# Optimization experiments

Measured on AMD Instinct MI355X. Metric: run time of the kernel, lower is better.

Reference implementation:

```python
import jax, jax.numpy as jnp
import numpy as np

N = 50000        # nodes
E = 1_600_000    # edges
G = 64           # graphs in batch
IN = 10          # raw node feature width
XS, XE = 4, 10   # bus slice -> in_dim = 6
H = 256          # hidden_dim
OUT = 256        # out_dim
L = 3            # n_layers per expert
NE = 8           # n_experts
K = 2            # top_k


def _w(key, shape):
    fan_in = shape[-2] if len(shape) > 1 else shape[-1]
    return jax.random.normal(key, shape, jnp.float32) / np.sqrt(fan_in).astype(np.float32)


def setup_inputs() -> dict:
    key = jax.random.key(0)
    ks = jax.random.split(key, 18)
    x = jax.random.normal(ks[0], (N, IN), jnp.float32)
    edge_index = jax.random.randint(ks[1], (2, E), 0, N, dtype=jnp.int32)
    batch = jnp.sort(jax.random.randint(ks[2], (N,), 0, G, dtype=jnp.int32))
    return {
        "x": x,
        "edge_index": edge_index,
        "batch": batch,
        # SharedBusEncoder: Linear(in_dim, hidden) + ReLU
        "W_enc": _w(ks[3], (XE - XS, H)), "b_enc": jnp.zeros((H,), jnp.float32),
        # semantic BaseRouter: Linear(H,H)+ReLU+Linear(H,NE)
        "Ws1": _w(ks[4], (H, H)), "bs1": jnp.zeros((H,), jnp.float32),
        "Ws2": _w(ks[5], (H, NE)), "bs2": jnp.zeros((NE,), jnp.float32),
        # structural BaseRouter: Linear(2,H)+ReLU+Linear(H,NE)
        "Wt1": _w(ks[6], (2, H)), "bt1": jnp.zeros((H,), jnp.float32),
        "Wt2": _w(ks[7], (H, NE)), "bt2": jnp.zeros((NE,), jnp.float32),
        # GraphConvExpert stacks: x' = x@W_self + (sum_neighbors x)@W_neigh + b
        "W_self": _w(ks[8], (NE, L, H, OUT)),
        "W_neigh": _w(ks[9], (NE, L, H, OUT)),
        "b_exp": jnp.zeros((NE, L, OUT), jnp.float32),
    }


def reference(x, edge_index, batch, W_enc, b_enc, Ws1, bs1, Ws2, bs2,
              Wt1, bt1, Wt2, bt2, W_self, W_neigh, b_exp):
    src, dst = edge_index[0], edge_index[1]

    # SharedBusEncoder on bus feature slice
    h = jax.nn.relu(x[:, XS:XE] @ W_enc + b_enc)                       # [N, H]

    # graph_size_features: per-graph log node/edge counts, broadcast to nodes
    nodes_per_g = jax.ops.segment_sum(jnp.ones((N,), jnp.float32), batch, G)
    edges_per_g = jax.ops.segment_sum(jnp.ones((E,), jnp.float32), batch[src], G)
    size_feat = jnp.stack([jnp.log1p(nodes_per_g), jnp.log1p(edges_per_g)], -1)[batch]  # [N, 2]

    # dual routers, averaged
    sem = jax.nn.relu(h @ Ws1 + bs1) @ Ws2 + bs2                       # [N, NE]
    stru = jax.nn.relu(size_feat @ Wt1 + bt1) @ Wt2 + bt2              # [N, NE]
    logits = 0.5 * sem + 0.5 * stru

    # sparse_routing: softmax -> top-k mask -> renormalize (eval path, no noise)
    probs = jax.nn.softmax(logits, axis=-1)
    _, topi = jax.lax.top_k(probs, K)                                  # [N, K]
    mask = jnp.zeros_like(probs).at[jnp.arange(N)[:, None], topi].set(1.0)
    sp = probs * mask
    sparse = sp / jnp.sum(sp, axis=-1, keepdims=True)                  # [N, NE]

    # dense GraphConv experts over all nodes
    def run_expert(Ws, Wn, b):
        z = h
        for l in range(L):
            agg = jax.ops.segment_sum(z[src], dst, N)                  # neighbor sum
            z = z @ Ws[l] + agg @ Wn[l] + b[l]
            if l < L - 1:
                z = jax.nn.relu(z)
        return z                                                        # [N, OUT]

    y = jax.vmap(run_expert)(W_self, W_neigh, b_exp)                   # [NE, N, OUT]
    return jnp.einsum('end,ne->nd', y, sparse)                         # [N, OUT]
```

## Files before the change

### kernel.cpp

```cpp
#include <hip/hip_runtime.h>
#include <hip/hip_bf16.h>


#define NN 50000
#define EE 1600000
#define GG 64
#define HH 256
#define NEXP 8
#define LAY 3
#define KD 512
#define MT 128
#define BK 64
#define LST 72

typedef __attribute__((ext_vector_type(8))) short bf16x8;
typedef __attribute__((ext_vector_type(8))) unsigned short u16x8;
typedef __attribute__((ext_vector_type(4))) float f32x4;

__device__ __forceinline__ float bf2f(unsigned short u) {
    union { unsigned int i; float f; } v; v.i = ((unsigned int)u) << 16; return v.f;
}
__device__ __forceinline__ unsigned short f2bf(float f) {
    union { unsigned int i; float f; } v; v.f = f;
    unsigned int r = (v.i + 0x7FFFu + ((v.i >> 16) & 1u)) >> 16;
    return (unsigned short)r;
}

__global__ void encoder_kernel(const float* __restrict__ x, const float* __restrict__ W,
                               const float* __restrict__ b, unsigned short* __restrict__ out) {
    int n = blockIdx.x, j = threadIdx.x;
    float acc = b[j];
#pragma unroll
    for (int i = 0; i < 6; i++) acc += x[n * 10 + 4 + i] * W[i * HH + j];
    acc = fmaxf(acc, 0.f);
    out[(long)n * KD + j] = f2bf(acc);
}

__global__ void pack_experts(const float* __restrict__ Wself, const float* __restrict__ Wneigh,
                             unsigned short* __restrict__ Bt) {
    int idx = blockIdx.x * 256 + threadIdx.x;
    int n = idx & 255; int r = idx >> 8;
    int k = r & 511; r >>= 9;
    int l = r % LAY; int e = r / LAY;
    float v = (k < 256) ? Wself[(((e * LAY + l) * HH) + k) * HH + n]
                        : Wneigh[(((e * LAY + l) * HH) + (k - 256)) * HH + n];
    Bt[(((long)(e * LAY + l) * HH + n) * KD) + k] = f2bf(v);
}

__global__ void pack_ws1(const float* __restrict__ W, unsigned short* __restrict__ Bt) {
    int idx = blockIdx.x * 256 + threadIdx.x;
    int n = idx & 255; int k = idx >> 8;
    Bt[(long)n * HH + k] = f2bf(W[k * HH + n]);
}

__global__ void deg_kernel(const int* __restrict__ src, const int* __restrict__ dst,
                           int* __restrict__ deg, int* __restrict__ outdeg) {
    int e = blockIdx.x * 256 + threadIdx.x;
    if (e < EE) {
        atomicAdd(&deg[dst[e]], 1);
        atomicAdd(&outdeg[src[e]], 1);
    }
}

__global__ void hist_kernel(const int* __restrict__ batch, const int* __restrict__ outdeg,
                            int* __restrict__ ncnt, int* __restrict__ ecnt) {
    __shared__ int hn[GG], he[GG];
    if (threadIdx.x < GG) { hn[threadIdx.x] = 0; he[threadIdx.x] = 0; }
    __syncthreads();
    int i = blockIdx.x * 256 + threadIdx.x;
    if (i < NN) {
        int g = batch[i];
        atomicAdd(&hn[g], 1);
        atomicAdd(&he[g], outdeg[i]);
    }
    __syncthreads();
    if (threadIdx.x < GG) {
        if (hn[threadIdx.x]) atomicAdd(&ncnt[threadIdx.x], hn[threadIdx.x]);
        if (he[threadIdx.x]) atomicAdd(&ecnt[threadIdx.x], he[threadIdx.x]);
    }
}

__global__ void stru_kernel(const int* __restrict__ ncnt, const int* __restrict__ ecnt,
                            const float* __restrict__ Wt1, const float* __restrict__ bt1,
                            const float* __restrict__ Wt2, const float* __restrict__ bt2,
                            float* __restrict__ strug) {
    __shared__ float t[HH];
    int g = blockIdx.x, j = threadIdx.x;
    float nf = log1pf((float)ncnt[g]);
    float ef = log1pf((float)ecnt[g]);
    float v = nf * Wt1[j] + ef * Wt1[HH + j] + bt1[j];
    t[j] = fmaxf(v, 0.f);
    __syncthreads();
    if (j < 8) {
        float sum = bt2[j];
        for (int k = 0; k < HH; k++) sum += t[k] * Wt2[k * 8 + j];
        strug[g * 8 + j] = sum;
    }
}

__global__ void scan_kernel(const int* __restrict__ deg, int* __restrict__ rowstart,
                            int* __restrict__ cursor) {
    __shared__ int wsum[16];
    __shared__ int carry_s;
    int tid = threadIdx.x;
    int wid = tid >> 6, lane = tid & 63;
    if (tid == 0) carry_s = 0;
    __syncthreads();
    for (int base = 0; base < NN; base += 1024) {
        int i = base + tid;
        int v = (i < NN) ? deg[i] : 0;
        int sc = v;
#pragma unroll
        for (int off = 1; off < 64; off <<= 1) {
            int t = __shfl_up(sc, off, 64);
            if (lane >= off) sc += t;
        }
        if (lane == 63) wsum[wid] = sc;
        __syncthreads();
        int carry = carry_s;
        int prev = 0;
        for (int w = 0; w < wid; w++) prev += wsum[w];
        int excl = carry + prev + sc - v;
        if (i < NN) { rowstart[i] = excl; cursor[i] = excl; }
        __syncthreads();
        if (tid == 1023) carry_s = carry + prev + sc;
    }
    __syncthreads();
    if (tid == 0) rowstart[NN] = carry_s;
}

__global__ void scatter_kernel(const int* __restrict__ src, const int* __restrict__ dst,
                               int* __restrict__ cursor, unsigned short* __restrict__ cols) {
    int e = blockIdx.x * 256 + threadIdx.x;
    if (e < EE) {
        int p = atomicAdd(&cursor[dst[e]], 1);
        cols[p] = (unsigned short)src[e];
    }
}

__global__ void agg_kernel(const unsigned short* __restrict__ Z, unsigned short* __restrict__ Aout,
                           const int* __restrict__ rowstart, const unsigned short* __restrict__ cols,
                           const int* __restrict__ list, const int* __restrict__ cntp) {
    int half = threadIdx.x >> 5;
    int lane = threadIdx.x & 31;
    int idx = blockIdx.x * 8 + half;
    int limit = cntp ? *cntp : NN;
    if (idx >= limit) return;
    int nid = list ? list[idx] : idx;
    int s = rowstart[nid], e = rowstart[nid + 1];
    float acc[8] = {0.f, 0.f, 0.f, 0.f, 0.f, 0.f, 0.f, 0.f};
    int i = s;
    for (; i + 8 <= e; i += 8) {
        int c[8];
#pragma unroll
        for (int u = 0; u < 8; u++) c[u] = (int)cols[i + u];
        u16x8 v[8];
#pragma unroll
        for (int u = 0; u < 8; u++) v[u] = *(const u16x8*)&Z[(long)c[u] * KD + lane * 8];
#pragma unroll
        for (int u = 0; u < 8; u++)
#pragma unroll
            for (int j = 0; j < 8; j++) acc[j] += bf2f(v[u][j]);
    }
    for (; i < e; i++) {
        int c = (int)cols[i];
        u16x8 v = *(const u16x8*)&Z[(long)c * KD + lane * 8];
#pragma unroll
        for (int j = 0; j < 8; j++) acc[j] += bf2f(v[j]);
    }
    u16x8 o;
#pragma unroll
    for (int j = 0; j < 8; j++) o[j] = f2bf(acc[j]);
    *(u16x8*)&Aout[(long)nid * KD + 256 + lane * 8] = o;
}

__global__ void route_kernel(const unsigned short* __restrict__ T, const float* __restrict__ Ws2,
                             const float* __restrict__ bs2, const float* __restrict__ strug,
                             const int* __restrict__ batch, float* __restrict__ sparse) {
    int nid = blockIdx.x * 4 + (threadIdx.x >> 6);
    if (nid >= NN) return;
    int lane = threadIdx.x & 63;
    float s[8];
#pragma unroll
    for (int j = 0; j < 8; j++) s[j] = 0.f;
    ushort4 t4 = *(const ushort4*)&T[(long)nid * HH + lane * 4];
    float tv[4] = { bf2f(t4.x), bf2f(t4.y), bf2f(t4.z), bf2f(t4.w) };
#pragma unroll
    for (int kk = 0; kk < 4; kk++) {
        int k = lane * 4 + kk;
#pragma unroll
        for (int j = 0; j < 8; j++) s[j] += tv[kk] * Ws2[k * 8 + j];
    }
#pragma unroll
    for (int off = 32; off >= 1; off >>= 1) {
#pragma unroll
        for (int j = 0; j < 8; j++) s[j] += __shfl_xor(s[j], off, 64);
    }
    int g = batch[nid];
    float p[8], mx = -1e30f;
#pragma unroll
    for (int j = 0; j < 8; j++) {
        p[j] = 0.5f * (s[j] + bs2[j] + strug[g * 8 + j]);
        mx = fmaxf(mx, p[j]);
    }
    float ex[8];
#pragma unroll
    for (int j = 0; j < 8; j++) ex[j] = expf(p[j] - mx);
    int i1 = 0;
#pragma unroll
    for (int j = 1; j < 8; j++) if (ex[j] > ex[i1]) i1 = j;
    int i2 = (i1 == 0) ? 1 : 0;
#pragma unroll
    for (int j = 0; j < 8; j++) if (j != i1 && ex[j] > ex[i2]) i2 = j;
    float r = 1.f / (ex[i1] + ex[i2]);
    if (lane < 8)
        sparse[(long)nid * 8 + lane] = (lane == i1) ? ex[i1] * r : (lane == i2) ? ex[i2] * r : 0.f;
}

__global__ void build_lists(const float* __restrict__ sparse, int* __restrict__ cnt,
                            int* __restrict__ lists) {
    int n = blockIdx.x * 256 + threadIdx.x;
    if (n >= NN) return;
#pragma unroll
    for (int e = 0; e < NEXP; e++) {
        if (sparse[n * 8 + e] > 0.f) {
            int p = atomicAdd(&cnt[e], 1);
            lists[(long)e * NN + p] = n;
        }
    }
}

template <int MODE>
__global__ __launch_bounds__(256, 2) void gemm_kernel(
    const unsigned short* __restrict__ A, int lda, int K,
    const unsigned short* __restrict__ Bt, const float* __restrict__ bias,
    void* __restrict__ outp, int ldz,
    const float* __restrict__ sparse, int expert,
    const int* __restrict__ list, const int* __restrict__ cntp) {
    __shared__ __align__(16) unsigned short Alds[MT * LST];
    __shared__ __align__(16) unsigned short Blds[HH * LST];
    __shared__ int nodeids[MT];
    const int tid = threadIdx.x;
    const int wave = tid >> 6, lane = tid & 63;
    const int m = lane & 15, q = lane >> 4;
    const long row0 = (long)blockIdx.x * MT;

    if constexpr (MODE == 1) {
        int limit = *cntp;
        if (row0 >= limit) return;
        if (tid < MT) {
            long rr = row0 + tid;
            nodeids[tid] = (rr < limit) ? list[rr] : -1;
        }
        __syncthreads();
    }

    f32x4 acc[2][16];
#pragma unroll
    for (int i = 0; i < 2; i++)
#pragma unroll
        for (int j = 0; j < 16; j++) acc[i][j] = (f32x4){0.f, 0.f, 0.f, 0.f};

    for (int k0 = 0; k0 < K; k0 += BK) {
#pragma unroll
        for (int i = 0; i < 4; i++) {
            int chunk = tid + 256 * i;
            int r = chunk >> 3, kc = (chunk & 7) << 3;
            u16x8 v = {0, 0, 0, 0, 0, 0, 0, 0};
            if constexpr (MODE == 0) {
                long grow = row0 + r;
                if (grow < NN) v = *(const u16x8*)&A[grow * lda + k0 + kc];
            } else {
                int nid2 = nodeids[r];
                if (nid2 >= 0) v = *(const u16x8*)&A[(long)nid2 * lda + k0 + kc];
            }
            *(u16x8*)&Alds[r * LST + kc] = v;
        }
#pragma unroll
        for (int i = 0; i < 8; i++) {
            int chunk = tid + 256 * i;
            int nn2 = chunk >> 3, kc = (chunk & 7) << 3;
            u16x8 v = *(const u16x8*)&Bt[(long)nn2 * K + k0 + kc];
            *(u16x8*)&Blds[nn2 * LST + kc] = v;
        }
        __syncthreads();
#pragma unroll
        for (int kk = 0; kk < BK; kk += 32) {
            bf16x8 a0 = *(const bf16x8*)&Alds[(wave * 32 + m) * LST + kk + q * 8];
            bf16x8 a1 = *(const bf16x8*)&Alds[(wave * 32 + 16 + m) * LST + kk + q * 8];
#pragma unroll
            for (int ct = 0; ct < 16; ct++) {
                bf16x8 b = *(const bf16x8*)&Blds[(ct * 16 + m) * LST + kk + q * 8];
                acc[0][ct] = __builtin_amdgcn_mfma_f32_16x16x32_bf16(a0, b, acc[0][ct], 0, 0, 0);
                acc[1][ct] = __builtin_amdgcn_mfma_f32_16x16x32_bf16(a1, b, acc[1][ct], 0, 0, 0);
            }
        }
        __syncthreads();
    }
#pragma unroll
    for (int mt = 0; mt < 2; mt++) {
        int rtile = wave * 32 + mt * 16 + q * 4;
        if constexpr (MODE == 0) {
            long rbase = row0 + rtile;
#pragma unroll
            for (int ct = 0; ct < 16; ct++) {
                int col = ct * 16 + m;
                float bv = bias[col];
#pragma unroll
                for (int r = 0; r < 4; r++) {
                    long grow = rbase + r;
                    if (grow < NN) {
                        float v = fmaxf(acc[mt][ct][r] + bv, 0.f);
                        ((unsigned short*)outp)[grow * ldz + col] = f2bf(v);
                    }
                }
            }
        } else {
            int nid4[4]; float w4[4];
#pragma unroll
            for (int r = 0; r < 4; r++) {
                nid4[r] = nodeids[rtile + r];
                w4[r] = (nid4[r] >= 0) ? sparse[(long)nid4[r] * 8 + expert] : 0.f;
            }
#pragma unroll
            for (int ct = 0; ct < 16; ct++) {
                int col = ct * 16 + m;
                float bv = bias[col];
#pragma unroll
                for (int r = 0; r < 4; r++) {
                    if (nid4[r] >= 0) {
                        float* o = (float*)outp + (long)nid4[r] * HH + col;
                        *o += w4[r] * (acc[mt][ct][r] + bv);
                    }
                }
            }
        }
    }
}

extern "C" void kernel_launch(void* const* d_in, const int* in_sizes, int n_in,
                              void* d_out, int out_size, void* d_ws, size_t ws_size,
                              hipStream_t stream) {
    const float* x     = (const float*)d_in[0];
    const int*   ei    = (const int*)d_in[1];
    const int*   src   = ei;
    const int*   dst   = ei + EE;
    const int*   batch = (const int*)d_in[2];
    const float* W_enc = (const float*)d_in[3];
    const float* b_enc = (const float*)d_in[4];
    const float* Ws1   = (const float*)d_in[5];
    const float* bs1   = (const float*)d_in[6];
    const float* Ws2   = (const float*)d_in[7];
    const float* bs2   = (const float*)d_in[8];
    const float* Wt1   = (const float*)d_in[9];
    const float* bt1   = (const float*)d_in[10];
    const float* Wt2   = (const float*)d_in[11];
    const float* bt2   = (const float*)d_in[12];
    const float* W_self  = (const float*)d_in[13];
    const float* W_neigh = (const float*)d_in[14];
    const float* b_exp   = (const float*)d_in[15];
    float* out = (float*)d_out;

    char* ws = (char*)d_ws;
    size_t off = 0;
    auto alloc = [&](size_t b) { size_t p = off; off = (off + b + 255) & ~(size_t)255; return p; };
    const size_t MPAD = 50048;

    unsigned short* Ash = (unsigned short*)(ws + alloc(MPAD * KD * 2));
    unsigned short* Ab0 = (unsigned short*)(ws + alloc(MPAD * KD * 2));
    unsigned short* Ab1 = (unsigned short*)(ws + alloc(MPAD * KD * 2));
    unsigned short* Tbuf = Ab1;
    unsigned short* BtE = (unsigned short*)(ws + alloc((size_t)NEXP * LAY * HH * KD * 2));
    unsigned short* Bt1 = (unsigned short*)(ws + alloc((size_t)HH * HH * 2));
    float* sparse  = (float*)(ws + alloc((size_t)NN * 8 * 4));
    float* strug   = (float*)(ws + alloc((size_t)GG * 8 * 4));
    int* ncnt      = (int*)(ws + alloc((size_t)GG * 4));
    int* ecnt      = (int*)(ws + alloc((size_t)GG * 4));
    int* deg       = (int*)(ws + alloc((size_t)NN * 4));
    int* outdeg    = (int*)(ws + alloc((size_t)NN * 4));
    int* rowstart  = (int*)(ws + alloc((size_t)(NN + 1) * 4));
    int* cursor    = (int*)(ws + alloc((size_t)NN * 4));
    unsigned short* cols = (unsigned short*)(ws + alloc((size_t)EE * 2));
    int* lists     = (int*)(ws + alloc((size_t)NEXP * NN * 4));
    int* cnt8      = (int*)(ws + alloc((size_t)NEXP * 4));

    hipMemsetAsync(ncnt, 0, GG * 4, stream);
    hipMemsetAsync(ecnt, 0, GG * 4, stream);
    hipMemsetAsync(deg, 0, (size_t)NN * 4, stream);
    hipMemsetAsync(outdeg, 0, (size_t)NN * 4, stream);
    hipMemsetAsync(cnt8, 0, NEXP * 4, stream);
    hipMemsetAsync(out, 0, (size_t)NN * HH * 4, stream);

    pack_experts<<<NEXP * LAY * KD * HH / 256, 256, 0, stream>>>(W_self, W_neigh, BtE);
    pack_ws1<<<HH * HH / 256, 256, 0, stream>>>(Ws1, Bt1);
    encoder_kernel<<<NN, HH, 0, stream>>>(x, W_enc, b_enc, Ash);

    deg_kernel<<<(EE + 255) / 256, 256, 0, stream>>>(src, dst, deg, outdeg);
    hist_kernel<<<(NN + 255) / 256, 256, 0, stream>>>(batch, outdeg, ncnt, ecnt);
    scan_kernel<<<1, 1024, 0, stream>>>(deg, rowstart, cursor);
    scatter_kernel<<<(EE + 255) / 256, 256, 0, stream>>>(src, dst, cursor, cols);
    stru_kernel<<<GG, HH, 0, stream>>>(ncnt, ecnt, Wt1, bt1, Wt2, bt2, strug);

    const int GB = (NN + MT - 1) / MT;
    const int AGB = NN / 8;

    gemm_kernel<0><<<GB, 256, 0, stream>>>(Ash, KD, HH, Bt1, bs1, Tbuf, HH, nullptr, 0,
                                           nullptr, nullptr);
    route_kernel<<<(NN + 3) / 4, 256, 0, stream>>>(Tbuf, Ws2, bs2, strug, batch, sparse);
    build_lists<<<(NN + 255) / 256, 256, 0, stream>>>(sparse, cnt8, lists);

    agg_kernel<<<AGB, 256, 0, stream>>>(Ash, Ash, rowstart, cols, nullptr, nullptr);

    for (int e = 0; e < NEXP; e++) {
        const unsigned short* B0 = BtE + (size_t)(e * LAY + 0) * HH * KD;
        const unsigned short* B1 = BtE + (size_t)(e * LAY + 1) * HH * KD;
        const unsigned short* B2 = BtE + (size_t)(e * LAY + 2) * HH * KD;
        const float* bb = b_exp + (size_t)e * LAY * HH;
        const int* le = lists + (size_t)e * NN;
        gemm_kernel<0><<<GB, 256, 0, stream>>>(Ash, KD, KD, B0, bb, Ab0, KD, nullptr, 0,
                                               nullptr, nullptr);
        agg_kernel<<<AGB, 256, 0, stream>>>(Ab0, Ab0, rowstart, cols, nullptr, nullptr);
        gemm_kernel<0><<<GB, 256, 0, stream>>>(Ab0, KD, KD, B1, bb + HH, Ab1, KD, nullptr, 0,
                                               nullptr, nullptr);
        agg_kernel<<<AGB, 256, 0, stream>>>(Ab1, Ab1, rowstart, cols, le, cnt8 + e);
        gemm_kernel<1><<<GB, 256, 0, stream>>>(Ab1, KD, KD, B2, bb + 2 * HH, out, 0, sparse, e,
                                               le, cnt8 + e);
    }
}
```

Before: 2.462 ms.

## Batch experts across grid dimension and stream GEMM tiles via global_load_lds

Processes groups of experts in one launch by indexing expert buffers, weights and biases through blockIdx.y, sizing the group to fit the available workspace. The GEMM now loads A and B tiles straight into LDS with global_load_lds, using an XOR swizzle in place of row padding. It also drops the output memset and the fp32 read-modify-write accumulation: each node's top-1 and top-2 weighted expert results go into separate bf16 planes, and a final combine kernel adds them. The CSR build records per-edge slot ranks during the degree pass, which removes the cursor atomics in the scatter. Node counts per graph come from a binary search over the sorted batch array. The trade-offs are more workspace, the intermediate result rounded to bf16, and some layers computed in place.

```diff
diff --git a/kernel.cpp b/kernel.cpp
--- a/kernel.cpp
+++ b/kernel.cpp
@@ -1,5 +1,4 @@
 #include <hip/hip_runtime.h>
-#include <hip/hip_bf16.h>
 
 
 #define NN 50000
@@ -11,7 +10,9 @@
 #define KD 512
 #define MT 128
 #define BK 64
-#define LST 72
+#define GB 391
+#define AGB 6250
+#define MPAD 50048L
 
 typedef __attribute__((ext_vector_type(8))) short bf16x8;
 typedef __attribute__((ext_vector_type(8))) unsigned short u16x8;
@@ -24,6 +25,10 @@
     union { unsigned int i; float f; } v; v.f = f;
     unsigned int r = (v.i + 0x7FFFu + ((v.i >> 16) & 1u)) >> 16;
     return (unsigned short)r;
+}
+__device__ __forceinline__ void gll16(unsigned short* l, const unsigned short* g) {
+    __builtin_amdgcn_global_load_lds((__attribute__((address_space(1))) void*)g,
+                                     (__attribute__((address_space(3))) void*)l, 16, 0, 0);
 }
 
 __global__ void encoder_kernel(const float* __restrict__ x, const float* __restrict__ W,
@@ -53,40 +58,37 @@
     Bt[(long)n * HH + k] = f2bf(W[k * HH + n]);
 }
 
-__global__ void deg_kernel(const int* __restrict__ src, const int* __restrict__ dst,
-                           int* __restrict__ deg, int* __restrict__ outdeg) {
+__global__ void deg2_kernel(const int* __restrict__ src, const int* __restrict__ dst,
+                            const int* __restrict__ batch, int* __restrict__ deg,
+                            unsigned short* __restrict__ perm, int* __restrict__ ecnt) {
+    __shared__ int he[GG];
+    if (threadIdx.x < GG) he[threadIdx.x] = 0;
+    __syncthreads();
     int e = blockIdx.x * 256 + threadIdx.x;
     if (e < EE) {
-        atomicAdd(&deg[dst[e]], 1);
-        atomicAdd(&outdeg[src[e]], 1);
-    }
-}
-
-__global__ void hist_kernel(const int* __restrict__ batch, const int* __restrict__ outdeg,
-                            int* __restrict__ ncnt, int* __restrict__ ecnt) {
-    __shared__ int hn[GG], he[GG];
-    if (threadIdx.x < GG) { hn[threadIdx.x] = 0; he[threadIdx.x] = 0; }
-    __syncthreads();
-    int i = blockIdx.x * 256 + threadIdx.x;
-    if (i < NN) {
-        int g = batch[i];
-        atomicAdd(&hn[g], 1);
-        atomicAdd(&he[g], outdeg[i]);
-    }
-    __syncthreads();
-    if (threadIdx.x < GG) {
-        if (hn[threadIdx.x]) atomicAdd(&ncnt[threadIdx.x], hn[threadIdx.x]);
-        if (he[threadIdx.x]) atomicAdd(&ecnt[threadIdx.x], he[threadIdx.x]);
-    }
-}
-
-__global__ void stru_kernel(const int* __restrict__ ncnt, const int* __restrict__ ecnt,
+        perm[e] = (unsigned short)atomicAdd(&deg[dst[e]], 1);
+        atomicAdd(&he[batch[src[e]]], 1);
+    }
+    __syncthreads();
+    if (threadIdx.x < GG && he[threadIdx.x]) atomicAdd(&ecnt[threadIdx.x], he[threadIdx.x]);
+}
+
+__global__ void stru_kernel(const int* __restrict__ batch, const int* __restrict__ ecnt,
                             const float* __restrict__ Wt1, const float* __restrict__ bt1,
                             const float* __restrict__ Wt2, const float* __restrict__ bt2,
                             float* __restrict__ strug) {
     __shared__ float t[HH];
+    __shared__ int nc;
     int g = blockIdx.x, j = threadIdx.x;
-    float nf = log1pf((float)ncnt[g]);
+    if (j == 0) {
+        int lo = 0, hi = NN;
+        while (lo < hi) { int mid = (lo + hi) >> 1; if (batch[mid] < g) lo = mid + 1; else hi = mid; }
+        int s = lo; lo = 0; hi = NN;
+        while (lo < hi) { int mid = (lo + hi) >> 1; if (batch[mid] < g + 1) lo = mid + 1; else hi = mid; }
+        nc = lo - s;
+    }
+    __syncthreads();
+    float nf = log1pf((float)nc);
     float ef = log1pf((float)ecnt[g]);
     float v = nf * Wt1[j] + ef * Wt1[HH + j] + bt1[j];
     t[j] = fmaxf(v, 0.f);
@@ -98,8 +100,7 @@
     }
 }
 
-__global__ void scan_kernel(const int* __restrict__ deg, int* __restrict__ rowstart,
-                            int* __restrict__ cursor) {
+__global__ void scan_kernel(const int* __restrict__ deg, int* __restrict__ rowstart) {
     __shared__ int wsum[16];
     __shared__ int carry_s;
     int tid = threadIdx.x;
@@ -121,7 +122,7 @@
         int prev = 0;
         for (int w = 0; w < wid; w++) prev += wsum[w];
         int excl = carry + prev + sc - v;
-        if (i < NN) { rowstart[i] = excl; cursor[i] = excl; }
+        if (i < NN) rowstart[i] = excl;
         __syncthreads();
         if (tid == 1023) carry_s = carry + prev + sc;
     }
@@ -129,24 +130,25 @@
     if (tid == 0) rowstart[NN] = carry_s;
 }
 
-__global__ void scatter_kernel(const int* __restrict__ src, const int* __restrict__ dst,
-                               int* __restrict__ cursor, unsigned short* __restrict__ cols) {
+__global__ void scatter2_kernel(const int* __restrict__ src, const int* __restrict__ dst,
+                                const unsigned short* __restrict__ perm,
+                                const int* __restrict__ rowstart,
+                                unsigned short* __restrict__ cols) {
     int e = blockIdx.x * 256 + threadIdx.x;
-    if (e < EE) {
-        int p = atomicAdd(&cursor[dst[e]], 1);
-        cols[p] = (unsigned short)src[e];
-    }
-}
-
-__global__ void agg_kernel(const unsigned short* __restrict__ Z, unsigned short* __restrict__ Aout,
+    if (e < EE) cols[rowstart[dst[e]] + (int)perm[e]] = (unsigned short)src[e];
+}
+
+__global__ void agg_kernel(unsigned short* __restrict__ base, long estride,
                            const int* __restrict__ rowstart, const unsigned short* __restrict__ cols,
-                           const int* __restrict__ list, const int* __restrict__ cntp) {
+                           const int* __restrict__ listp, const int* __restrict__ cntp) {
+    const unsigned short* Z = base + (long)blockIdx.y * estride;
+    unsigned short* Aout = base + (long)blockIdx.y * estride;
     int half = threadIdx.x >> 5;
     int lane = threadIdx.x & 31;
     int idx = blockIdx.x * 8 + half;
-    int limit = cntp ? *cntp : NN;
+    int limit = cntp ? cntp[blockIdx.y] : NN;
     if (idx >= limit) return;
-    int nid = list ? list[idx] : idx;
+    int nid = listp ? (listp[(long)blockIdx.y * NN + idx] & 0xFFFF) : idx;
     int s = rowstart[nid], e = rowstart[nid + 1];
     float acc[8] = {0.f, 0.f, 0.f, 0.f, 0.f, 0.f, 0.f, 0.f};
     int i = s;
@@ -176,7 +178,8 @@
 
 __global__ void route_kernel(const unsigned short* __restrict__ T, const float* __restrict__ Ws2,
                              const float* __restrict__ bs2, const float* __restrict__ strug,
-                             const int* __restrict__ batch, float* __restrict__ sparse) {
+                             const int* __restrict__ batch, float* __restrict__ sparse,
+                             int* __restrict__ topi) {
     int nid = blockIdx.x * 4 + (threadIdx.x >> 6);
     if (nid >= NN) return;
     int lane = threadIdx.x & 63;
@@ -213,84 +216,113 @@
 #pragma unroll
     for (int j = 0; j < 8; j++) if (j != i1 && ex[j] > ex[i2]) i2 = j;
     float r = 1.f / (ex[i1] + ex[i2]);
+    if (lane == 0) topi[nid] = i1 | (i2 << 8);
     if (lane < 8)
         sparse[(long)nid * 8 + lane] = (lane == i1) ? ex[i1] * r : (lane == i2) ? ex[i2] * r : 0.f;
 }
 
-__global__ void build_lists(const float* __restrict__ sparse, int* __restrict__ cnt,
-                            int* __restrict__ lists) {
-    int n = blockIdx.x * 256 + threadIdx.x;
-    if (n >= NN) return;
-#pragma unroll
-    for (int e = 0; e < NEXP; e++) {
-        if (sparse[n * 8 + e] > 0.f) {
-            int p = atomicAdd(&cnt[e], 1);
-            lists[(long)e * NN + p] = n;
-        }
-    }
+__global__ void build_lists(const float* __restrict__ sparse, const int* __restrict__ topi,
+                            int* __restrict__ cnt, int* __restrict__ lists) {
+    __shared__ int lc[NEXP], lb[NEXP];
+    int tid = threadIdx.x;
+    if (tid < NEXP) lc[tid] = 0;
+    __syncthreads();
+    int n = blockIdx.x * 256 + tid;
+    int le_[2], pk_[2], ps_[2];
+    int cc = 0;
+    if (n < NN) {
+        int t1 = topi[n] & 0xFF;
+#pragma unroll
+        for (int e = 0; e < NEXP; e++) {
+            if (sparse[(long)n * 8 + e] > 0.f && cc < 2) {
+                le_[cc] = e;
+                pk_[cc] = n | ((e == t1) ? 0 : (1 << 16));
+                ps_[cc] = atomicAdd(&lc[e], 1);
+                cc++;
+            }
+        }
+    }
+    __syncthreads();
+    if (tid < NEXP) lb[tid] = atomicAdd(&cnt[tid], lc[tid]);
+    __syncthreads();
+    for (int c = 0; c < cc; c++)
+        lists[(long)le_[c] * NN + lb[le_[c]] + ps_[c]] = pk_[c];
 }
 
 template <int MODE>
 __global__ __launch_bounds__(256, 2) void gemm_kernel(
-    const unsigned short* __restrict__ A, int lda, int K,
-    const unsigned short* __restrict__ Bt, const float* __restrict__ bias,
-    void* __restrict__ outp, int ldz,
-    const float* __restrict__ sparse, int expert,
-    const int* __restrict__ list, const int* __restrict__ cntp) {
-    __shared__ __align__(16) unsigned short Alds[MT * LST];
-    __shared__ __align__(16) unsigned short Blds[HH * LST];
+    const unsigned short* __restrict__ A, long ae, int lda, int K,
+    const unsigned short* __restrict__ Bt, long bte,
+    const float* __restrict__ bias, int be_s,
+    void* __restrict__ outp, long oe, int ldz,
+    const float* __restrict__ sparse, int e0,
+    const int* __restrict__ listp, const int* __restrict__ cntp) {
+    __shared__ __align__(16) unsigned short Alds[MT * 64];
+    __shared__ __align__(16) unsigned short Blds[HH * 64];
     __shared__ int nodeids[MT];
+    const int el = blockIdx.y;
+    const unsigned short* Ae = A + (long)el * ae;
+    const unsigned short* Bte = Bt + (long)el * bte;
+    const float* be = bias + (long)el * be_s;
     const int tid = threadIdx.x;
     const int wave = tid >> 6, lane = tid & 63;
     const int m = lane & 15, q = lane >> 4;
     const long row0 = (long)blockIdx.x * MT;
 
     if constexpr (MODE == 1) {
-        int limit = *cntp;
+        int limit = cntp[el];
         if (row0 >= limit) return;
         if (tid < MT) {
             long rr = row0 + tid;
-            nodeids[tid] = (rr < limit) ? list[rr] : -1;
+            nodeids[tid] = (rr < limit) ? listp[(long)el * NN + rr] : -1;
         }
         __syncthreads();
     }
 
+    const unsigned short* asrc[4];
+#pragma unroll
+    for (int i = 0; i < 4; i++) {
+        int slot = tid + 256 * i;
+        int r = slot >> 3, cg = (slot & 7) ^ (r & 7);
+        long arow;
+        if constexpr (MODE == 0) {
+            arow = row0 + r;
+        } else {
+            int v = nodeids[r];
+            arow = (v >= 0) ? (v & 0xFFFF) : 0;
+        }
+        asrc[i] = Ae + arow * (long)lda + cg * 8;
+    }
+    const unsigned short* bsrc[8];
+#pragma unroll
+    for (int i = 0; i < 8; i++) {
+        int slot = tid + 256 * i;
+        int r = slot >> 3, cg = (slot & 7) ^ (r & 7);
+        bsrc[i] = Bte + (long)r * K + cg * 8;
+    }
+
     f32x4 acc[2][16];
 #pragma unroll
     for (int i = 0; i < 2; i++)
 #pragma unroll
         for (int j = 0; j < 16; j++) acc[i][j] = (f32x4){0.f, 0.f, 0.f, 0.f};
 
+    const int swz = (m & 7) << 3;
     for (int k0 = 0; k0 < K; k0 += BK) {
 #pragma unroll
-        for (int i = 0; i < 4; i++) {
-            int chunk = tid + 256 * i;
-            int r = chunk >> 3, kc = (chunk & 7) << 3;
-            u16x8 v = {0, 0, 0, 0, 0, 0, 0, 0};
-            if constexpr (MODE == 0) {
-                long grow = row0 + r;
-                if (grow < NN) v = *(const u16x8*)&A[grow * lda + k0 + kc];
-            } else {
-                int nid2 = nodeids[r];
-                if (nid2 >= 0) v = *(const u16x8*)&A[(long)nid2 * lda + k0 + kc];
-            }
-            *(u16x8*)&Alds[r * LST + kc] = v;
-        }
-#pragma unroll
-        for (int i = 0; i < 8; i++) {
-            int chunk = tid + 256 * i;
-            int nn2 = chunk >> 3, kc = (chunk & 7) << 3;
-            u16x8 v = *(const u16x8*)&Bt[(long)nn2 * K + k0 + kc];
-            *(u16x8*)&Blds[nn2 * LST + kc] = v;
-        }
+        for (int i = 0; i < 4; i++) gll16(&Alds[(tid + 256 * i) * 8], asrc[i] + k0);
+#pragma unroll
+        for (int i = 0; i < 8; i++) gll16(&Blds[(tid + 256 * i) * 8], bsrc[i] + k0);
         __syncthreads();
 #pragma unroll
         for (int kk = 0; kk < BK; kk += 32) {
-            bf16x8 a0 = *(const bf16x8*)&Alds[(wave * 32 + m) * LST + kk + q * 8];
-            bf16x8 a1 = *(const bf16x8*)&Alds[(wave * 32 + 16 + m) * LST + kk + q * 8];
+            const int ch8 = (((kk >> 3) + q) << 3) ^ swz;
+            const int ao = (wave * 32 + m) * 64 + ch8;
+            bf16x8 a0 = *(const bf16x8*)&Alds[ao];
+            bf16x8 a1 = *(const bf16x8*)&Alds[ao + 16 * 64];
 #pragma unroll
             for (int ct = 0; ct < 16; ct++) {
-                bf16x8 b = *(const bf16x8*)&Blds[(ct * 16 + m) * LST + kk + q * 8];
+                bf16x8 b = *(const bf16x8*)&Blds[(ct * 16 + m) * 64 + ch8];
                 acc[0][ct] = __builtin_amdgcn_mfma_f32_16x16x32_bf16(a0, b, acc[0][ct], 0, 0, 0);
                 acc[1][ct] = __builtin_amdgcn_mfma_f32_16x16x32_bf16(a1, b, acc[1][ct], 0, 0, 0);
             }
@@ -301,41 +333,57 @@
     for (int mt = 0; mt < 2; mt++) {
         int rtile = wave * 32 + mt * 16 + q * 4;
         if constexpr (MODE == 0) {
+            unsigned short* oute = (unsigned short*)outp + (long)el * oe;
             long rbase = row0 + rtile;
 #pragma unroll
             for (int ct = 0; ct < 16; ct++) {
                 int col = ct * 16 + m;
-                float bv = bias[col];
+                float bv = be[col];
 #pragma unroll
                 for (int r = 0; r < 4; r++) {
                     long grow = rbase + r;
                     if (grow < NN) {
                         float v = fmaxf(acc[mt][ct][r] + bv, 0.f);
-                        ((unsigned short*)outp)[grow * ldz + col] = f2bf(v);
+                        oute[grow * ldz + col] = f2bf(v);
                     }
                 }
             }
         } else {
-            int nid4[4]; float w4[4];
+            unsigned short* outR = (unsigned short*)outp;
+            int v4[4]; float w4[4];
 #pragma unroll
             for (int r = 0; r < 4; r++) {
-                nid4[r] = nodeids[rtile + r];
-                w4[r] = (nid4[r] >= 0) ? sparse[(long)nid4[r] * 8 + expert] : 0.f;
+                v4[r] = nodeids[rtile + r];
+                w4[r] = (v4[r] >= 0) ? sparse[(long)(v4[r] & 0xFFFF) * 8 + e0 + el] : 0.f;
             }
 #pragma unroll
             for (int ct = 0; ct < 16; ct++) {
                 int col = ct * 16 + m;
-                float bv = bias[col];
+                float bv = be[col];
 #pragma unroll
                 for (int r = 0; r < 4; r++) {
-                    if (nid4[r] >= 0) {
-                        float* o = (float*)outp + (long)nid4[r] * HH + col;
-                        *o += w4[r] * (acc[mt][ct][r] + bv);
+                    if (v4[r] >= 0) {
+                        long nid = v4[r] & 0xFFFF;
+                        long rank = (v4[r] >> 16) & 1;
+                        outR[(rank * MPAD + nid) * HH + col] = f2bf(w4[r] * (acc[mt][ct][r] + bv));
                     }
                 }
             }
         }
     }
+}
+
+__global__ void combine_kernel(const unsigned short* __restrict__ outR, float* __restrict__ out) {
+    long base = ((long)blockIdx.x * 256 + threadIdx.x) * 8;
+    u16x8 r0 = *(const u16x8*)&outR[base];
+    u16x8 r1 = *(const u16x8*)&outR[MPAD * HH + base];
+    f32x4 lo, hi;
+#pragma unroll
+    for (int j = 0; j < 4; j++) lo[j] = bf2f(r0[j]) + bf2f(r1[j]);
+#pragma unroll
+    for (int j = 0; j < 4; j++) hi[j] = bf2f(r0[j + 4]) + bf2f(r1[j + 4]);
+    *(f32x4*)&out[base] = lo;
+    *(f32x4*)&out[base + 4] = hi;
 }
 
 extern "C" void kernel_launch(void* const* d_in, const int* in_sizes, int n_in,
@@ -363,67 +411,69 @@
 
     char* ws = (char*)d_ws;
     size_t off = 0;
-    auto alloc = [&](size_t b) { size_t p = off; off = (off + b + 255) & ~(size_t)255; return p; };
-    const size_t MPAD = 50048;
-
-    unsigned short* Ash = (unsigned short*)(ws + alloc(MPAD * KD * 2));
-    unsigned short* Ab0 = (unsigned short*)(ws + alloc(MPAD * KD * 2));
-    unsigned short* Ab1 = (unsigned short*)(ws + alloc(MPAD * KD * 2));
-    unsigned short* Tbuf = Ab1;
-    unsigned short* BtE = (unsigned short*)(ws + alloc((size_t)NEXP * LAY * HH * KD * 2));
-    unsigned short* Bt1 = (unsigned short*)(ws + alloc((size_t)HH * HH * 2));
-    float* sparse  = (float*)(ws + alloc((size_t)NN * 8 * 4));
-    float* strug   = (float*)(ws + alloc((size_t)GG * 8 * 4));
-    int* ncnt      = (int*)(ws + alloc((size_t)GG * 4));
-    int* ecnt      = (int*)(ws + alloc((size_t)GG * 4));
-    int* deg       = (int*)(ws + alloc((size_t)NN * 4));
-    int* outdeg    = (int*)(ws + alloc((size_t)NN * 4));
-    int* rowstart  = (int*)(ws + alloc((size_t)(NN + 1) * 4));
-    int* cursor    = (int*)(ws + alloc((size_t)NN * 4));
-    unsigned short* cols = (unsigned short*)(ws + alloc((size_t)EE * 2));
-    int* lists     = (int*)(ws + alloc((size_t)NEXP * NN * 4));
-    int* cnt8      = (int*)(ws + alloc((size_t)NEXP * 4));
-
-    hipMemsetAsync(ncnt, 0, GG * 4, stream);
+    auto alloc = [&](size_t b) { size_t p = off; off = (off + b + 255) & ~(size_t)255; return ws + p; };
+
+    unsigned short* Ash  = (unsigned short*)alloc((size_t)MPAD * KD * 2);
+    unsigned short* outR = (unsigned short*)alloc((size_t)2 * MPAD * HH * 2);
+    unsigned short* Tbuf = outR;
+    unsigned short* BtE = (unsigned short*)alloc((size_t)NEXP * LAY * HH * KD * 2);
+    unsigned short* Bt1 = (unsigned short*)alloc((size_t)HH * HH * 2);
+    float* sparse  = (float*)alloc((size_t)NN * 8 * 4);
+    int* topi      = (int*)alloc((size_t)NN * 4);
+    float* strug   = (float*)alloc((size_t)GG * 8 * 4);
+    int* ecnt      = (int*)alloc((size_t)GG * 4);
+    int* deg       = (int*)alloc((size_t)NN * 4);
+    int* rowstart  = (int*)alloc((size_t)(NN + 1) * 4);
+    unsigned short* perm = (unsigned short*)alloc((size_t)EE * 2);
+    unsigned short* cols = (unsigned short*)alloc((size_t)EE * 2);
+    int* lists     = (int*)alloc((size_t)NEXP * NN * 4);
+    int* cnt8      = (int*)alloc((size_t)NEXP * 4);
+
+    const long BUFS = MPAD * KD;
+    long avail = ((long)ws_size - (long)off) / (BUFS * 2);
+    int EG = (avail < 1) ? 1 : (avail > NEXP ? NEXP : (int)avail);
+    unsigned short* bufs = (unsigned short*)(ws + off);
+
     hipMemsetAsync(ecnt, 0, GG * 4, stream);
     hipMemsetAsync(deg, 0, (size_t)NN * 4, stream);
-    hipMemsetAsync(outdeg, 0, (size_t)NN * 4, stream);
     hipMemsetAsync(cnt8, 0, NEXP * 4, stream);
-    hipMemsetAsync(out, 0, (size_t)NN * HH * 4, stream);
 
     pack_experts<<<NEXP * LAY * KD * HH / 256, 256, 0, stream>>>(W_self, W_neigh, BtE);
     pack_ws1<<<HH * HH / 256, 256, 0, stream>>>(Ws1, Bt1);
     encoder_kernel<<<NN, HH, 0, stream>>>(x, W_enc, b_enc, Ash);
 
-    deg_kernel<<<(EE + 255) / 256, 256, 0, stream>>>(src, dst, deg, outdeg);
-    hist_kernel<<<(NN + 255) / 256, 256, 0, stream>>>(batch, outdeg, ncnt, ecnt);
-    scan_kernel<<<1, 1024, 0, stream>>>(deg, rowstart, cursor);
-    scatter_kernel<<<(EE + 255) / 256, 256, 0, stream>>>(src, dst, cursor, cols);
-    stru_kernel<<<GG, HH, 0, stream>>>(ncnt, ecnt, Wt1, bt1, Wt2, bt2, strug);
-
-    const int GB = (NN + MT - 1) / MT;
-    const int AGB = NN / 8;
-
-    gemm_kernel<0><<<GB, 256, 0, stream>>>(Ash, KD, HH, Bt1, bs1, Tbuf, HH, nullptr, 0,
-                                           nullptr, nullptr);
-    route_kernel<<<(NN + 3) / 4, 256, 0, stream>>>(Tbuf, Ws2, bs2, strug, batch, sparse);
-    build_lists<<<(NN + 255) / 256, 256, 0, stream>>>(sparse, cnt8, lists);
-
-    agg_kernel<<<AGB, 256, 0, stream>>>(Ash, Ash, rowstart, cols, nullptr, nullptr);
-
-    for (int e = 0; e < NEXP; e++) {
-        const unsigned short* B0 = BtE + (size_t)(e * LAY + 0) * HH * KD;
-        const unsigned short* B1 = BtE + (size_t)(e * LAY + 1) * HH * KD;
-        const unsigned short* B2 = BtE + (size_t)(e * LAY + 2) * HH * KD;
-        const float* bb = b_exp + (size_t)e * LAY * HH;
-        const int* le = lists + (size_t)e * NN;
-        gemm_kernel<0><<<GB, 256, 0, stream>>>(Ash, KD, KD, B0, bb, Ab0, KD, nullptr, 0,
-                                               nullptr, nullptr);
-        agg_kernel<<<AGB, 256, 0, stream>>>(Ab0, Ab0, rowstart, cols, nullptr, nullptr);
-        gemm_kernel<0><<<GB, 256, 0, stream>>>(Ab0, KD, KD, B1, bb + HH, Ab1, KD, nullptr, 0,
-                                               nullptr, nullptr);
-        agg_kernel<<<AGB, 256, 0, stream>>>(Ab1, Ab1, rowstart, cols, le, cnt8 + e);
-        gemm_kernel<1><<<GB, 256, 0, stream>>>(Ab1, KD, KD, B2, bb + 2 * HH, out, 0, sparse, e,
-                                               le, cnt8 + e);
-    }
-}
+    deg2_kernel<<<(EE + 255) / 256, 256, 0, stream>>>(src, dst, batch, deg, perm, ecnt);
+    scan_kernel<<<1, 1024, 0, stream>>>(deg, rowstart);
+    scatter2_kernel<<<(EE + 255) / 256, 256, 0, stream>>>(src, dst, perm, rowstart, cols);
+    stru_kernel<<<GG, HH, 0, stream>>>(batch, ecnt, Wt1, bt1, Wt2, bt2, strug);
+
+    gemm_kernel<0><<<dim3(GB, 1), 256, 0, stream>>>(Ash, 0, KD, HH, Bt1, 0, bs1, 0,
+                                                    Tbuf, 0, HH, nullptr, 0, nullptr, nullptr);
+    route_kernel<<<(NN + 3) / 4, 256, 0, stream>>>(Tbuf, Ws2, bs2, strug, batch, sparse, topi);
+    build_lists<<<(NN + 255) / 256, 256, 0, stream>>>(sparse, topi, cnt8, lists);
+
+    agg_kernel<<<dim3(AGB, 1), 256, 0, stream>>>(Ash, 0, rowstart, cols, nullptr, nullptr);
+
+    const long BTL = (long)LAY * HH * KD;
+    for (int e0 = 0; e0 < NEXP; e0 += EG) {
+        int eg = (NEXP - e0 < EG) ? (NEXP - e0) : EG;
+        dim3 gg(GB, eg), ga(AGB, eg);
+        gemm_kernel<0><<<gg, 256, 0, stream>>>(Ash, 0, KD, KD,
+                                               BtE + (size_t)(e0 * LAY + 0) * HH * KD, BTL,
+                                               b_exp + (size_t)e0 * LAY * HH, LAY * HH,
+                                               bufs, BUFS, KD, nullptr, 0, nullptr, nullptr);
+        agg_kernel<<<ga, 256, 0, stream>>>(bufs, BUFS, rowstart, cols, nullptr, nullptr);
+        gemm_kernel<0><<<gg, 256, 0, stream>>>(bufs, BUFS, KD, KD,
+                                               BtE + (size_t)(e0 * LAY + 1) * HH * KD, BTL,
+                                               b_exp + (size_t)e0 * LAY * HH + HH, LAY * HH,
+                                               bufs, BUFS, KD, nullptr, 0, nullptr, nullptr);
+        agg_kernel<<<ga, 256, 0, stream>>>(bufs, BUFS, rowstart, cols,
+                                           lists + (size_t)e0 * NN, cnt8 + e0);
+        gemm_kernel<1><<<gg, 256, 0, stream>>>(bufs, BUFS, KD, KD,
+                                               BtE + (size_t)(e0 * LAY + 2) * HH * KD, BTL,
+                                               b_exp + (size_t)e0 * LAY * HH + 2 * HH, LAY * HH,
+                                               outR, 0, 0, sparse, e0,
+                                               lists + (size_t)e0 * NN, cnt8 + e0);
+    }
+    combine_kernel<<<NN * HH / 8 / 256, 256, 0, stream>>>(outR, out);
+}
```

Measured after the change: 2.168 ms. 11.9% less time.
